# Optimization experiments

Hardware: AMD Instinct MI355X
Metric: run time of the kernel (lower is better)

## Reference

```python
import jax, jax.numpy as jnp
import numpy as np

N_WIRES = 8
DIM = 2 ** N_WIRES  # 256


def _rx(theta):
    # theta: [] or [N] -> [2,2] or [N,2,2] complex64
    c = jnp.cos(theta / 2)
    s = jnp.sin(theta / 2)
    return jnp.stack([jnp.stack([c + 0j, -1j * s], -1),
                      jnp.stack([-1j * s, c + 0j], -1)], -2)


def _ry(theta):
    c = jnp.cos(theta / 2)
    s = jnp.sin(theta / 2)
    return jnp.stack([jnp.stack([c + 0j, -s + 0j], -1),
                      jnp.stack([s + 0j, c + 0j], -1)], -2)


def _rz(theta):
    e = jnp.exp(-1j * theta / 2)
    z = jnp.zeros_like(e)
    return jnp.stack([jnp.stack([e, z], -1),
                      jnp.stack([z, jnp.conj(e)], -1)], -2)


def _apply_1q(state, U, wire):
    # state: [N, DIM]; U: [2,2] (shared) or [N,2,2] (per-sample)
    s = state.reshape(-1, 2 ** wire, 2, 2 ** (N_WIRES - 1 - wire))
    if U.ndim == 2:
        s = jnp.einsum('ab,nxby->nxay', U, s)
    else:
        s = jnp.einsum('nab,nxby->nxay', U, s)
    return s.reshape(-1, DIM)


def _cnot(state, c, t):
    # wire 0 = most significant bit (PennyLane convention)
    s = state.reshape((-1,) + (2,) * N_WIRES)
    ax_c = 1 + c
    s0 = jnp.take(s, 0, axis=ax_c)
    s1 = jnp.take(s, 1, axis=ax_c)
    ax_t = 1 + t if t < c else t  # target axis after control axis removed
    s1 = jnp.flip(s1, axis=ax_t)
    s = jnp.stack([s0, s1], axis=ax_c)
    return s.reshape(-1, DIM)


def _z_signs():
    idx = np.arange(DIM)
    bits = (idx[:, None] >> (N_WIRES - 1 - np.arange(N_WIRES))[None, :]) & 1
    return jnp.asarray(1.0 - 2.0 * bits, dtype=jnp.float32)  # [DIM, 8]


def _circuit(x_flat, params):
    # x_flat: [N, 8] angles; params: [8, 3]
    n = x_flat.shape[0]
    state = jnp.zeros((n, DIM), dtype=jnp.complex64).at[:, 0].set(1.0)
    for i in range(N_WIRES):
        state = _apply_1q(state, _rx(x_flat[:, i]), i)
    for i in range(N_WIRES):
        state = _apply_1q(state, _ry(params[i, 0]), i)
        state = _apply_1q(state, _rz(params[i, 1]), i)
        state = _apply_1q(state, _rx(params[i, 2]), i)
    for i in range(N_WIRES - 1):
        state = _cnot(state, i, i + 1)
    state = _cnot(state, N_WIRES - 1, 0)
    probs = state.real ** 2 + state.imag ** 2  # [N, DIM]
    return probs @ _z_signs()  # [N, 8] PauliZ expvals


def setup_inputs() -> dict:
    key = jax.random.key(0)
    ks = jax.random.split(key, 4)
    B, S = 16, 2048
    embed_dim, ffn_dim = 512, 2048
    return {
        'x': jax.random.normal(ks[0], (B, S, N_WIRES), dtype=jnp.float32),
        'params': jax.random.normal(ks[1], (N_WIRES, 3), dtype=jnp.float32),
        'W1': jax.random.normal(ks[2], (ffn_dim, N_WIRES), dtype=jnp.float32) * 0.1,
        'b1': jnp.zeros((ffn_dim,), dtype=jnp.float32),
        'W2': jax.random.normal(ks[3], (embed_dim, ffn_dim), dtype=jnp.float32) * 0.02,
        'b2': jnp.zeros((embed_dim,), dtype=jnp.float32),
    }


def reference(x, params, W1, b1, W2, b2):
    B, S, _ = x.shape
    ev = _circuit(x.reshape(-1, N_WIRES), params).reshape(B, S, N_WIRES)
    h = jax.nn.relu(ev @ W1.T + b1)
    return h @ W2.T + b2
```

## Files before the change

kernel.cpp:

```cpp
#include <hip/hip_runtime.h>
#include <hip/hip_bf16.h>

#define NS 32768
#define EMB 512
#define KDIM 2048

typedef float f32x16 __attribute__((ext_vector_type(16)));
typedef __bf16 bf16x8 __attribute__((ext_vector_type(8)));
typedef __bf16 bf16x2 __attribute__((ext_vector_type(2)));
typedef unsigned int u32;
typedef const __attribute__((address_space(1))) u32* gptr_t;
typedef __attribute__((address_space(3))) u32* lptr_t;

#if __has_builtin(__builtin_amdgcn_fdot2_f32_bf16)
#define HAS_FDOT2 1
#else
#define HAS_FDOT2 0
#endif

__device__ __forceinline__ void gload_lds16(const void* g, void* l) {
    __builtin_amdgcn_global_load_lds((gptr_t)g, (lptr_t)l, 16, 0, 0);
}

__global__ __launch_bounds__(256) void k_prep(const float* __restrict__ W2,
                                              const float* __restrict__ W1,
                                              __hip_bfloat16* __restrict__ W2b,
                                              __hip_bfloat16* __restrict__ W1bg) {
    int t = threadIdx.x;
    if (blockIdx.x < 1024) {
        int i = (blockIdx.x * 256 + t) * 4;
        float4 v = *(const float4*)(W2 + i);
        __hip_bfloat16 o[4];
        o[0] = __float2bfloat16(v.x); o[1] = __float2bfloat16(v.y);
        o[2] = __float2bfloat16(v.z); o[3] = __float2bfloat16(v.w);
        *(ulong1*)(W2b + i) = *(ulong1*)o;
    } else {
        int j = (blockIdx.x - 1024) * 1024 + t * 4;
        float4 w = *(const float4*)(W1 + j);
        __hip_bfloat16 p[4];
        p[0] = __float2bfloat16(w.x); p[1] = __float2bfloat16(w.y);
        p[2] = __float2bfloat16(w.z); p[3] = __float2bfloat16(w.w);
        *(ulong1*)(W1bg + j) = *(ulong1*)p;
    }
}

#define BM 128
#define BN 256

__global__ __launch_bounds__(256, 2) void k_gemm(
        const float* __restrict__ x,
        const float* __restrict__ params,
        const __hip_bfloat16* __restrict__ W1bg,
        const float* __restrict__ b1,
        const __hip_bfloat16* __restrict__ W2b,
        const float* __restrict__ b2,
        float* __restrict__ C) {
    __shared__ __hip_bfloat16 Bs[16 * 512];
    __shared__ __hip_bfloat16 W1s[KDIM * 8];
    __shared__ float b1s[KDIM];
    __shared__ __hip_bfloat16 evs[BM * 8];

    int tid = threadIdx.x, wave = tid >> 6, lane = tid & 63;
    int l31 = lane & 31, half = lane >> 5;
    int bx = blockIdx.x, bm = bx >> 1, bn = bx & 1;

    if (tid < 128) {
        float K1[8], K2[8];
        #pragma unroll
        for (int i = 0; i < 8; i++) {
            float a = params[i*3+0], b = params[i*3+1], g = params[i*3+2];
            float sa, ca, sb, cb, sg, cg;
            __sincosf(a, &sa, &ca);
            __sincosf(b, &sb, &cb);
            __sincosf(g, &sg, &cg);
            K1[i] = sa*sb*sg + ca*cg;
            K2[i] = cb*sg;
        }
        int n = bm * BM + tid;
        float4 x0 = *(const float4*)(x + (size_t)n*8);
        float4 x1 = *(const float4*)(x + (size_t)n*8 + 4);
        float xs[8] = {x0.x, x0.y, x0.z, x0.w, x1.x, x1.y, x1.z, x1.w};
        float z[8];
        #pragma unroll
        for (int i = 0; i < 8; i++) {
            float s, c;
            __sincosf(xs[i], &s, &c);
            z[i] = c * K1[i] - s * K2[i];
        }
        float evv[8];
        float p = z[0];
        #pragma unroll
        for (int j = 1; j < 8; j++) { p *= z[j]; evv[j] = p; }
        float sfx = z[7];
        #pragma unroll
        for (int j = 6; j >= 1; j--) sfx *= z[j];
        evv[0] = sfx;
        __hip_bfloat16 o[8];
        #pragma unroll
        for (int i = 0; i < 8; i++) o[i] = __float2bfloat16(evv[i]);
        *(bf16x8*)&evs[tid * 8] = *(bf16x8*)o;
    }
    for (int i = tid; i < KDIM; i += 256) {
        *(bf16x8*)&W1s[i * 8] = *(const bf16x8*)(W1bg + (size_t)i * 8);
        b1s[i] = b1[i];
    }
    __syncthreads();

    bf16x8 evr = *(const bf16x8*)&evs[(wave * 32 + l31) * 8];
#if HAS_FDOT2
    bf16x2 ep[4];
    #pragma unroll
    for (int p = 0; p < 4; p++) ep[p] = (bf16x2){evr[2*p], evr[2*p+1]};
#else
    float ef[8];
    #pragma unroll
    for (int i = 0; i < 8; i++) ef[i] = (float)evr[i];
#endif

    const __hip_bfloat16* gBp[4];
    #pragma unroll
    for (int i = 0; i < 4; i++) {
        int f = wave * 4 + i, ni = f >> 1, t = f & 1;
        gBp[i] = W2b + (size_t)(bn*BN + ni*32 + l31) * KDIM + t*16 + half*8;
    }

    f32x16 acc[8] = {};

    for (int k0 = 0; k0 < KDIM; k0 += 32) {
        #pragma unroll
        for (int i = 0; i < 4; i++) {
            gload_lds16(gBp[i], &Bs[(wave*4 + i) * 512]);
            gBp[i] += 32;
        }
        __syncthreads();

        #pragma unroll
        for (int t = 0; t < 2; t++) {
            int kb = k0 + t*16 + half*8;
            float4 ba = *(const float4*)&b1s[kb];
            float4 bb = *(const float4*)&b1s[kb + 4];
            float bv[8] = {ba.x, ba.y, ba.z, ba.w, bb.x, bb.y, bb.z, bb.w};
            bf16x8 af;
            #pragma unroll
            for (int j = 0; j < 8; j++) {
                bf16x8 w = *(const bf16x8*)&W1s[(kb + j) * 8];
                float a = bv[j];
#if HAS_FDOT2
                #pragma unroll
                for (int p = 0; p < 4; p++) {
                    bf16x2 wp = (bf16x2){w[2*p], w[2*p+1]};
                    a = __builtin_amdgcn_fdot2_f32_bf16(ep[p], wp, a, false);
                }
#else
                #pragma unroll
                for (int i = 0; i < 8; i++) a = fmaf(ef[i], (float)w[i], a);
#endif
                af[j] = (__bf16)fmaxf(a, 0.f);
            }
            #pragma unroll
            for (int ni = 0; ni < 8; ni++) {
                bf16x8 bfr = *(const bf16x8*)&Bs[(ni*2 + t) * 512 + lane * 8];
                acc[ni] = __builtin_amdgcn_mfma_f32_32x32x16_bf16(
                              af, bfr, acc[ni], 0, 0, 0);
            }
        }
        __syncthreads();
    }

    int rbase = bm*BM + wave*32 + 4*half;
    #pragma unroll
    for (int ni = 0; ni < 8; ni++) {
        int col = bn*BN + ni*32 + l31;
        float bias = b2[col];
        #pragma unroll
        for (int r = 0; r < 16; r++) {
            int row = rbase + (r & 3) + 8 * (r >> 2);
            C[(size_t)row * EMB + col] = acc[ni][r] + bias;
        }
    }
}

extern "C" void kernel_launch(void* const* d_in, const int* in_sizes, int n_in,
                              void* d_out, int out_size, void* d_ws, size_t ws_size,
                              hipStream_t stream) {
    const float* x      = (const float*)d_in[0];
    const float* params = (const float*)d_in[1];
    const float* W1     = (const float*)d_in[2];
    const float* b1     = (const float*)d_in[3];
    const float* W2     = (const float*)d_in[4];
    const float* b2     = (const float*)d_in[5];
    float* out = (float*)d_out;

    char* ws = (char*)d_ws;
    __hip_bfloat16* W2b  = (__hip_bfloat16*)ws;
    __hip_bfloat16* W1bg = (__hip_bfloat16*)(ws + 2097152);

    k_prep<<<1040, 256, 0, stream>>>(W2, W1, W2b, W1bg);
    k_gemm<<<(NS/BM) * (EMB/BN), 256, 0, stream>>>(x, params, W1bg, b1, W2b, b2, out);
}
```

Measured before the change: 177.4 us.

## Compute hidden layer with MFMA and double-buffer W2 tiles in LDS

```diff
diff --git a/kernel.cpp b/kernel.cpp
--- a/kernel.cpp
+++ b/kernel.cpp
@@ -4,22 +4,39 @@
 #define NS 32768
 #define EMB 512
 #define KDIM 2048
+#define BM 128
+#define BN 256
+#define NITER (KDIM / 32)
 
 typedef float f32x16 __attribute__((ext_vector_type(16)));
 typedef __bf16 bf16x8 __attribute__((ext_vector_type(8)));
 typedef __bf16 bf16x2 __attribute__((ext_vector_type(2)));
 typedef unsigned int u32;
+typedef unsigned int u32x2 __attribute__((ext_vector_type(2)));
 typedef const __attribute__((address_space(1))) u32* gptr_t;
 typedef __attribute__((address_space(3))) u32* lptr_t;
 
-#if __has_builtin(__builtin_amdgcn_fdot2_f32_bf16)
-#define HAS_FDOT2 1
+#if __has_builtin(__builtin_amdgcn_permlane32_swap)
+#define HAS_PLS 1
 #else
-#define HAS_FDOT2 0
+#define HAS_PLS 0
 #endif
 
 __device__ __forceinline__ void gload_lds16(const void* g, void* l) {
     __builtin_amdgcn_global_load_lds((gptr_t)g, (lptr_t)l, 16, 0, 0);
+}
+
+__device__ __forceinline__ u32 pkrelu(float lo, float hi) {
+    union { bf16x2 h; u32 u; } c;
+    c.h[0] = (__bf16)fmaxf(lo, 0.f);
+    c.h[1] = (__bf16)fmaxf(hi, 0.f);
+    return c.u;
+}
+
+__device__ __forceinline__ bf16x8 mk_af(u32 a, u32 b, u32 c, u32 d) {
+    union { u32 u[4]; bf16x8 v; } t;
+    t.u[0] = a; t.u[1] = b; t.u[2] = c; t.u[3] = d;
+    return t.v;
 }
 
 __global__ __launch_bounds__(256) void k_prep(const float* __restrict__ W2,
@@ -44,9 +61,6 @@
     }
 }
 
-#define BM 128
-#define BN 256
-
 __global__ __launch_bounds__(256, 2) void k_gemm(
         const float* __restrict__ x,
         const float* __restrict__ params,
@@ -55,7 +69,7 @@
         const __hip_bfloat16* __restrict__ W2b,
         const float* __restrict__ b2,
         float* __restrict__ C) {
-    __shared__ __hip_bfloat16 Bs[16 * 512];
+    __shared__ __hip_bfloat16 Bs[2][16 * 512];
     __shared__ __hip_bfloat16 W1s[KDIM * 8];
     __shared__ float b1s[KDIM];
     __shared__ __hip_bfloat16 evs[BM * 8];
@@ -104,18 +118,6 @@
         *(bf16x8*)&W1s[i * 8] = *(const bf16x8*)(W1bg + (size_t)i * 8);
         b1s[i] = b1[i];
     }
-    __syncthreads();
-
-    bf16x8 evr = *(const bf16x8*)&evs[(wave * 32 + l31) * 8];
-#if HAS_FDOT2
-    bf16x2 ep[4];
-    #pragma unroll
-    for (int p = 0; p < 4; p++) ep[p] = (bf16x2){evr[2*p], evr[2*p+1]};
-#else
-    float ef[8];
-    #pragma unroll
-    for (int i = 0; i < 8; i++) ef[i] = (float)evr[i];
-#endif
 
     const __hip_bfloat16* gBp[4];
     #pragma unroll
@@ -123,47 +125,75 @@
         int f = wave * 4 + i, ni = f >> 1, t = f & 1;
         gBp[i] = W2b + (size_t)(bn*BN + ni*32 + l31) * KDIM + t*16 + half*8;
     }
+    #pragma unroll
+    for (int i = 0; i < 4; i++) {
+        gload_lds16(gBp[i], &Bs[0][(wave*4 + i) * 512]);
+        gBp[i] += 32;
+    }
+
+    __syncthreads();
+
+    bf16x8 evB = *(bf16x8*)&evs[(wave * 32 + l31) * 8];
 
     f32x16 acc[8] = {};
 
-    for (int k0 = 0; k0 < KDIM; k0 += 32) {
-        #pragma unroll
-        for (int i = 0; i < 4; i++) {
-            gload_lds16(gBp[i], &Bs[(wave*4 + i) * 512]);
-            gBp[i] += 32;
-        }
-        __syncthreads();
-
-        #pragma unroll
-        for (int t = 0; t < 2; t++) {
-            int kb = k0 + t*16 + half*8;
-            float4 ba = *(const float4*)&b1s[kb];
-            float4 bb = *(const float4*)&b1s[kb + 4];
-            float bv[8] = {ba.x, ba.y, ba.z, ba.w, bb.x, bb.y, bb.z, bb.w};
-            bf16x8 af;
+    for (int it = 0; it < NITER; ++it) {
+        const int k0 = it * 32;
+        const int cb = it & 1;
+
+        if (it + 1 < NITER) {
             #pragma unroll
-            for (int j = 0; j < 8; j++) {
-                bf16x8 w = *(const bf16x8*)&W1s[(kb + j) * 8];
-                float a = bv[j];
-#if HAS_FDOT2
-                #pragma unroll
-                for (int p = 0; p < 4; p++) {
-                    bf16x2 wp = (bf16x2){w[2*p], w[2*p+1]};
-                    a = __builtin_amdgcn_fdot2_f32_bf16(ep[p], wp, a, false);
-                }
+            for (int i = 0; i < 4; i++) {
+                gload_lds16(gBp[i], &Bs[cb ^ 1][(wave*4 + i) * 512]);
+                gBp[i] += 32;
+            }
+        }
+
+        bf16x8 w1f = {};
+        if (half == 0) w1f = *(const bf16x8*)&W1s[(k0 + l31) * 8];
+        float4 c0 = *(const float4*)&b1s[k0 + 4*half];
+        float4 c1 = *(const float4*)&b1s[k0 + 8 + 4*half];
+        float4 c2 = *(const float4*)&b1s[k0 + 16 + 4*half];
+        float4 c3 = *(const float4*)&b1s[k0 + 24 + 4*half];
+        f32x16 h;
+        h[0] = c0.x; h[1] = c0.y; h[2]  = c0.z; h[3]  = c0.w;
+        h[4] = c1.x; h[5] = c1.y; h[6]  = c1.z; h[7]  = c1.w;
+        h[8] = c2.x; h[9] = c2.y; h[10] = c2.z; h[11] = c2.w;
+        h[12] = c3.x; h[13] = c3.y; h[14] = c3.z; h[15] = c3.w;
+        h = __builtin_amdgcn_mfma_f32_32x32x16_bf16(w1f, evB, h, 0, 0, 0);
+
+        u32 w0  = pkrelu(h[0],  h[1]);  u32 w1v = pkrelu(h[2],  h[3]);
+        u32 wA  = pkrelu(h[4],  h[5]);  u32 wB  = pkrelu(h[6],  h[7]);
+        u32 w2v = pkrelu(h[8],  h[9]);  u32 w3v = pkrelu(h[10], h[11]);
+        u32 wC  = pkrelu(h[12], h[13]); u32 wD  = pkrelu(h[14], h[15]);
+#if HAS_PLS
+        { u32x2 r = __builtin_amdgcn_permlane32_swap(w0,  wA, false, false); w0  = r[0]; wA = r[1]; }
+        { u32x2 r = __builtin_amdgcn_permlane32_swap(w1v, wB, false, false); w1v = r[0]; wB = r[1]; }
+        { u32x2 r = __builtin_amdgcn_permlane32_swap(w2v, wC, false, false); w2v = r[0]; wC = r[1]; }
+        { u32x2 r = __builtin_amdgcn_permlane32_swap(w3v, wD, false, false); w3v = r[0]; wD = r[1]; }
+        bf16x8 af0 = mk_af(w0, w1v, wA, wB);
+        bf16x8 af1 = mk_af(w2v, w3v, wC, wD);
 #else
-                #pragma unroll
-                for (int i = 0; i < 8; i++) a = fmaf(ef[i], (float)w[i], a);
+        int pl = lane ^ 32;
+        u32 pw0 = __shfl((int)w0,  pl), pw1 = __shfl((int)w1v, pl);
+        u32 pwA = __shfl((int)wA,  pl), pwB = __shfl((int)wB,  pl);
+        u32 pw2 = __shfl((int)w2v, pl), pw3 = __shfl((int)w3v, pl);
+        u32 pwC = __shfl((int)wC,  pl), pwD = __shfl((int)wD,  pl);
+        bf16x8 af0 = half ? mk_af(pwA, pwB, wA, wB) : mk_af(w0,  w1v, pw0, pw1);
+        bf16x8 af1 = half ? mk_af(pwC, pwD, wC, wD) : mk_af(w2v, w3v, pw2, pw3);
 #endif
-                af[j] = (__bf16)fmaxf(a, 0.f);
-            }
-            #pragma unroll
-            for (int ni = 0; ni < 8; ni++) {
-                bf16x8 bfr = *(const bf16x8*)&Bs[(ni*2 + t) * 512 + lane * 8];
-                acc[ni] = __builtin_amdgcn_mfma_f32_32x32x16_bf16(
-                              af, bfr, acc[ni], 0, 0, 0);
-            }
-        }
+
+        #pragma unroll
+        for (int ni = 0; ni < 8; ni++) {
+            bf16x8 bfr = *(bf16x8*)&Bs[cb][(ni*2 + 0) * 512 + lane * 8];
+            acc[ni] = __builtin_amdgcn_mfma_f32_32x32x16_bf16(af0, bfr, acc[ni], 0, 0, 0);
+        }
+        #pragma unroll
+        for (int ni = 0; ni < 8; ni++) {
+            bf16x8 bfr = *(bf16x8*)&Bs[cb][(ni*2 + 1) * 512 + lane * 8];
+            acc[ni] = __builtin_amdgcn_mfma_f32_32x32x16_bf16(af1, bfr, acc[ni], 0, 0, 0);
+        }
+
         __syncthreads();
     }
 
```

Result: faster. 157.1 us (-11.4%).
